# Optimization experiments

Hardware: AMD Instinct MI355X
Metric: run time of the kernel (lower is better)

## Reference

```python
import jax, jax.numpy as jnp
import numpy as np

B, C, H, W = 16, 512, 32, 32
GROUPS = 8
EPS = 1e-5


def setup_inputs() -> dict:
    key = jax.random.key(0)
    ks = jax.random.split(key, 7)
    s = 1.0 / np.sqrt(C)
    return {
        "x": jax.random.normal(ks[0], (B, C, H, W), dtype=jnp.float32),
        "gamma": jnp.ones((C,), dtype=jnp.float32),
        "beta": jnp.zeros((C,), dtype=jnp.float32),
        "w_qkv": jax.random.normal(ks[1], (3 * C, C), dtype=jnp.float32) * s,
        "b_qkv": jnp.zeros((3 * C,), dtype=jnp.float32),
        "w_proj": jax.random.normal(ks[2], (C, C), dtype=jnp.float32) * s,
        "b_proj": jnp.zeros((C,), dtype=jnp.float32),
    }


def group_norm(x, gamma, beta):
    b, c, h, w = x.shape
    xg = x.reshape(b, GROUPS, c // GROUPS, h, w)
    mean = xg.mean(axis=(2, 3, 4), keepdims=True)
    var = xg.var(axis=(2, 3, 4), keepdims=True)
    xn = ((xg - mean) * jax.lax.rsqrt(var + EPS)).reshape(b, c, h, w)
    return xn * gamma[None, :, None, None] + beta[None, :, None, None]


def reference(x, gamma, beta, w_qkv, b_qkv, w_proj, b_proj):
    b, c, h, w = x.shape
    n = h * w
    hn = group_norm(x, gamma, beta)
    # 1x1 conv == channel matmul: [3C, C] x [B, C, N] -> [B, 3C, N]
    qkv = jnp.einsum('oc,bcn->bon', w_qkv, hn.reshape(b, c, n)) + b_qkv[None, :, None]
    q, k, v = jnp.split(qkv, 3, axis=1)  # each [B, C, N]
    scale = c ** (-0.5)
    # scores [B, N, N]: q^T k
    attn = jax.nn.softmax(jnp.einsum('bcn,bcm->bnm', q, k) * scale, axis=-1)
    out = jnp.einsum('bnm,bcm->bcn', attn, v)  # [B, C, N]
    proj = jnp.einsum('oc,bcn->bon', w_proj, out) + b_proj[None, :, None]
    return x + proj.reshape(b, c, h, w)
```

## Files before the change

kernel.cpp:

```cpp
#include <hip/hip_runtime.h>


#define BATCH 16
#define CCH 512
#define NSP 1024
#define EPSV 1e-5f
#define BK 32
#define HT 4096

typedef short bf16x8 __attribute__((ext_vector_type(8)));
typedef float f32x4 __attribute__((ext_vector_type(4)));

__device__ __forceinline__ unsigned short f2bf(float f) {
    unsigned int u = __float_as_uint(f);
    u += 0x7FFF + ((u >> 16) & 1);
    return (unsigned short)(u >> 16);
}

__device__ __forceinline__ float bf2f(unsigned short h) {
    return __uint_as_float(((unsigned int)h) << 16);
}

__device__ __forceinline__ void glds16(const void* g, void* l) {
    __builtin_amdgcn_global_load_lds(
        (const __attribute__((address_space(1))) unsigned int*)g,
        (__attribute__((address_space(3))) unsigned int*)l, 16, 0, 0);
}

#define MEMF asm volatile("" ::: "memory")
#define VMW(n) asm volatile("s_waitcnt vmcnt(" #n ")" ::: "memory")

#define XCD_MAP(GX_LOG2, PER, xv, yv, bv)                 \
    const int lin_ = blockIdx.x;                          \
    const int xcd_ = lin_ & 7;                            \
    int slot_ = lin_ >> 3;                                \
    const int hi_ = (slot_ >= (PER)) ? 1 : 0;             \
    const int bv = xcd_ + 8 * hi_;                        \
    slot_ -= hi_ * (PER);                                 \
    const int xv = slot_ & ((1 << (GX_LOG2)) - 1);        \
    const int yv = slot_ >> (GX_LOG2);

__device__ __forceinline__ void gemm128_dbuf(
    const unsigned short* __restrict__ Ag, const unsigned short* __restrict__ Bg,
    int astr, int bstr, int ktot, short* L, f32x4* acc) {
    const int t = threadIdx.x;
    const int w = t >> 6, lane = t & 63;
    const int wr = (w >> 1) * 64, wc = (w & 1) * 64;
    const int fr = lane & 15;
    const int fsw = (((lane >> 4) ^ (fr & 3)) * 8);
    const int r0 = t >> 2;
    const int kc = (((t & 3) ^ (r0 & 3)) * 8);
    const unsigned short* Ap0 = Ag + (size_t)r0 * astr + kc;
    const unsigned short* Ap1 = Ag + (size_t)(r0 + 64) * astr + kc;
    const unsigned short* Bp0 = Bg + (size_t)r0 * bstr + kc;
    const unsigned short* Bp1 = Bg + (size_t)(r0 + 64) * bstr + kc;
    short* lw = L + w * 512;

#define STG(bf, kk) do {                                  \
    short* aw_ = lw + (bf) * (4 * HT);                    \
    short* bw_ = aw_ + 2 * HT;                            \
    glds16(Ap0 + (kk), aw_);                              \
    glds16(Ap1 + (kk), aw_ + 2048);                       \
    glds16(Ap0 + (kk) + 32, aw_ + HT);                    \
    glds16(Ap1 + (kk) + 32, aw_ + HT + 2048);             \
    glds16(Bp0 + (kk), bw_);                              \
    glds16(Bp1 + (kk), bw_ + 2048);                       \
    glds16(Bp0 + (kk) + 32, bw_ + HT);                    \
    glds16(Bp1 + (kk) + 32, bw_ + HT + 2048);             \
  } while (0)

#define CMP(bf) do {                                                        \
    _Pragma("unroll")                                                       \
    for (int h = 0; h < 2; h++) {                                           \
        const short* Ab_ = L + (bf) * (4 * HT) + h * HT;                    \
        const short* Bb_ = Ab_ + 2 * HT;                                    \
        bf16x8 af[4], bfr[4];                                               \
        _Pragma("unroll")                                                   \
        for (int mi = 0; mi < 4; mi++)                                      \
            af[mi] = *(const bf16x8*)(Ab_ + (wr + mi * 16 + fr) * BK + fsw);\
        _Pragma("unroll")                                                   \
        for (int ni = 0; ni < 4; ni++)                                      \
            bfr[ni] = *(const bf16x8*)(Bb_ + (wc + ni * 16 + fr) * BK + fsw);\
        _Pragma("unroll")                                                   \
        for (int mi = 0; mi < 4; mi++)                                      \
            _Pragma("unroll")                                               \
            for (int ni = 0; ni < 4; ni++)                                  \
                acc[mi * 4 + ni] = __builtin_amdgcn_mfma_f32_16x16x32_bf16( \
                    af[mi], bfr[ni], acc[mi * 4 + ni], 0, 0, 0);            \
    } } while (0)

    STG(0, 0);
    for (int k0 = 0; k0 < ktot; k0 += 128) {
        STG(1, k0 + 64);
        VMW(8);
        MEMF; __builtin_amdgcn_s_barrier();
        CMP(0);
        MEMF; __builtin_amdgcn_s_barrier();
        const int kb = (k0 + 128 < ktot) ? k0 + 128 : 0;
        STG(0, kb);
        VMW(8);
        MEMF; __builtin_amdgcn_s_barrier();
        CMP(1);
        MEMF; __builtin_amdgcn_s_barrier();
    }
    VMW(0);
#undef STG
#undef CMP
}

__device__ __forceinline__ void gemm128_sb(
    const unsigned short* __restrict__ Ag, const unsigned short* __restrict__ Bg,
    int astr, int bstr, int ktot, short* Al, short* Bl, f32x4* acc) {
    const int t = threadIdx.x;
    const int w = t >> 6, lane = t & 63;
    const int wr = (w >> 1) * 64, wc = (w & 1) * 64;
    const int fr = lane & 15;
    const int fsw = (((lane >> 4) ^ (fr & 3)) * 8);
    const int r0 = t >> 2;
    const int kc = (((t & 3) ^ (r0 & 3)) * 8);
    const unsigned short* Ap0 = Ag + (size_t)r0 * astr + kc;
    const unsigned short* Ap1 = Ag + (size_t)(r0 + 64) * astr + kc;
    const unsigned short* Bp0 = Bg + (size_t)r0 * bstr + kc;
    const unsigned short* Bp1 = Bg + (size_t)(r0 + 64) * bstr + kc;
    short* Alw = Al + w * 512;
    short* Blw = Bl + w * 512;
    for (int k0 = 0; k0 < ktot; k0 += 64) {
        glds16(Ap0 + k0, Alw);
        glds16(Ap1 + k0, Alw + 2048);
        glds16(Ap0 + k0 + 32, Alw + HT);
        glds16(Ap1 + k0 + 32, Alw + HT + 2048);
        glds16(Bp0 + k0, Blw);
        glds16(Bp1 + k0, Blw + 2048);
        glds16(Bp0 + k0 + 32, Blw + HT);
        glds16(Bp1 + k0 + 32, Blw + HT + 2048);
        __syncthreads();
#pragma unroll
        for (int h = 0; h < 2; h++) {
            const short* Ab = Al + h * HT;
            const short* Bb = Bl + h * HT;
            bf16x8 af[4], bfr[4];
#pragma unroll
            for (int mi = 0; mi < 4; mi++)
                af[mi] = *(const bf16x8*)(Ab + (wr + mi * 16 + fr) * BK + fsw);
#pragma unroll
            for (int ni = 0; ni < 4; ni++)
                bfr[ni] = *(const bf16x8*)(Bb + (wc + ni * 16 + fr) * BK + fsw);
#pragma unroll
            for (int mi = 0; mi < 4; mi++)
#pragma unroll
                for (int ni = 0; ni < 4; ni++)
                    acc[mi * 4 + ni] = __builtin_amdgcn_mfma_f32_16x16x32_bf16(
                        af[mi], bfr[ni], acc[mi * 4 + ni], 0, 0, 0);
        }
        __syncthreads();
    }
}

#define EPI_SETUP()                                          \
    const int t = threadIdx.x, lane = t & 63, w = t >> 6;    \
    const int wr = (w >> 1) * 64, wc = (w & 1) * 64;         \
    const int fr = lane & 15, rr0 = (lane >> 4) * 4;

#define ACC_INIT(acc)                                        \
    f32x4 acc[16];                                           \
    _Pragma("unroll") for (int i = 0; i < 16; i++)           \
        acc[i] = (f32x4){0.f, 0.f, 0.f, 0.f};

__global__ __launch_bounds__(256) void setup_k(
    const float* __restrict__ x, float* __restrict__ sp,
    const float* __restrict__ wa, unsigned short* __restrict__ oa, int na4,
    const float* __restrict__ wb, unsigned short* __restrict__ ob, int nb4,
    float* __restrict__ Lsum, const float* __restrict__ bqv,
    unsigned short* __restrict__ wv_t, unsigned short* __restrict__ wq_t,
    unsigned short* __restrict__ wk_t, float* __restrict__ puv,
    float* __restrict__ wu, float* __restrict__ wv_b, float* __restrict__ c0p) {
    const int t = threadIdx.x;
    const int bx = blockIdx.x;
    __shared__ float rs[4], rq[4];
    __shared__ __align__(16) unsigned short Tt[64 * 72];
    if (bx < 512) {
        const int bg = bx >> 2, q = bx & 3;
        const float4* xp = (const float4*)(x + (size_t)bg * 65536 + q * 16384);
        float s = 0.f, qq = 0.f;
#pragma unroll
        for (int i = 0; i < 16; i++) {
            float4 v = xp[t + i * 256];
            s += v.x + v.y + v.z + v.w;
            qq += v.x * v.x + v.y * v.y + v.z * v.z + v.w * v.w;
        }
#pragma unroll
        for (int off = 32; off; off >>= 1) {
            s += __shfl_down(s, off);
            qq += __shfl_down(qq, off);
        }
        const int wave = t >> 6, lane = t & 63;
        if (lane == 0) { rs[wave] = s; rq[wave] = qq; }
        __syncthreads();
        if (t == 0) {
            sp[bx * 2] = rs[0] + rs[1] + rs[2] + rs[3];
            sp[bx * 2 + 1] = rq[0] + rq[1] + rq[2] + rq[3];
        }
    } else if (bx < 1280) {
        int i = (bx - 512) * 256 + t;
        const float* src;
        unsigned short* dst;
        int j;
        if (i < na4) { src = wa; dst = oa; j = i; }
        else { j = i - na4; if (j >= nb4) return; src = wb; dst = ob; }
        float4 v = ((const float4*)src)[j];
        ushort4 o;
        o.x = f2bf(v.x); o.y = f2bf(v.y); o.z = f2bf(v.z); o.w = f2bf(v.w);
        ((ushort4*)dst)[j] = o;
    } else if (bx < 1328) {
        int i = (bx - 1280) * 256 + t;
        ((float4*)Lsum)[i] = (float4){0.f, 0.f, 0.f, 0.f};
    } else if (bx < 1520) {
        const int r = bx - 1328;
        const int sel = r >> 6;
        const int wrow = (sel == 0) ? 2 : (sel - 1);
        const float* src = wa + (size_t)wrow * 512 * 512;
        unsigned short* dst = (sel == 0) ? wv_t : ((sel == 1) ? wq_t : wk_t);
        const int to = ((r & 63) >> 3) * 64, tc = ((r & 63) & 7) * 64;
        const int ol = t >> 2, cs = t & 3;
#pragma unroll
        for (int j = 0; j < 4; j++) {
            float4 v = *(const float4*)(src + (size_t)(to + ol) * 512 + tc + cs * 16 + j * 4);
            int c = cs * 16 + j * 4;
            Tt[(c + 0) * 72 + ol] = f2bf(v.x);
            Tt[(c + 1) * 72 + ol] = f2bf(v.y);
            Tt[(c + 2) * 72 + ol] = f2bf(v.z);
            Tt[(c + 3) * 72 + ol] = f2bf(v.w);
        }
        __syncthreads();
        const int cl = t >> 2, os = t & 3;
        unsigned short* d = dst + (size_t)(tc + cl) * 512 + to + os * 16;
        const unsigned short* s2 = Tt + cl * 72 + os * 16;
        *(uint4*)d = *(const uint4*)s2;
        *(uint4*)(d + 8) = *(const uint4*)(s2 + 8);
    } else if (bx < 1522) {
        const int o = (bx - 1520) * 256 + t;
        const float* wr_ = wb + (size_t)o * 512;
        const float* bv = bqv + 1024;
        float s = 0.f;
        for (int vv = 0; vv < 512; vv += 4) {
            s += wr_[vv] * bv[vv] + wr_[vv + 1] * bv[vv + 1]
               + wr_[vv + 2] * bv[vv + 2] + wr_[vv + 3] * bv[vv + 3];
        }
        puv[o] = s;
    } else if (bx < 1526) {
        const int r = bx - 1522;
        const int isv = r >> 1;
        const int c = (r & 1) * 256 + t;
        const float* src = wa + (size_t)isv * 512 * 512;
        const float* bsr = bqv + (isv ? 0 : 512);
        float s = 0.f;
        for (int o = 0; o < 512; o++) s += src[(size_t)o * 512 + c] * bsr[o];
        (isv ? wv_b : wu)[c] = s;
    } else {
        float s = bqv[t] * bqv[512 + t] + bqv[256 + t] * bqv[768 + t];
#pragma unroll
        for (int off = 32; off; off >>= 1) s += __shfl_down(s, off);
        if ((t & 63) == 0) rs[t >> 6] = s;
        __syncthreads();
        if (t == 0) c0p[0] = rs[0] + rs[1] + rs[2] + rs[3];
    }
}

__global__ __launch_bounds__(256) void gn_tr_k(
    const float* __restrict__ x, const float* __restrict__ gamma,
    const float* __restrict__ beta, const float* __restrict__ sp,
    unsigned short* __restrict__ hn_t,
    const unsigned short* __restrict__ wp_bf, const unsigned short* __restrict__ wv_t,
    unsigned short* __restrict__ wpv_bf,
    const unsigned short* __restrict__ wk_t, const unsigned short* __restrict__ wq_t,
    unsigned short* __restrict__ wqkb,
    const float* __restrict__ wu, const float* __restrict__ wv_b,
    float* __restrict__ u, float* __restrict__ v) {
    __shared__ __align__(16) short SM[4 * HT];
    const int lin = blockIdx.x;
    const int t = threadIdx.x;
    if (lin < 16) {
        const int ot = (lin >> 2) * 128, ct2 = (lin & 3) * 128;
        ACC_INIT(acc);
        gemm128_sb(wp_bf + (size_t)ot * 512, wv_t + (size_t)ct2 * 512,
                   512, 512, 512, SM, SM + 2 * HT, acc);
        EPI_SETUP();
#pragma unroll
        for (int ni = 0; ni < 4; ni++) {
            int col = ct2 + wc + ni * 16 + fr;
#pragma unroll
            for (int mi = 0; mi < 4; mi++) {
                int row = ot + wr + mi * 16 + rr0;
#pragma unroll
                for (int r = 0; r < 4; r++)
                    wpv_bf[(size_t)(row + r) * 512 + col] = f2bf(acc[mi * 4 + ni][r]);
            }
        }
        return;
    }
    if (lin < 32) {
        const int r2 = lin - 16;
        const int jt = (r2 >> 2) * 128, ct2 = (r2 & 3) * 128;
        ACC_INIT(acc);
        gemm128_sb(wk_t + (size_t)jt * 512, wq_t + (size_t)ct2 * 512,
                   512, 512, 512, SM, SM + 2 * HT, acc);
        EPI_SETUP();
#pragma unroll
        for (int ni = 0; ni < 4; ni++) {
            int col = ct2 + wc + ni * 16 + fr;
#pragma unroll
            for (int mi = 0; mi < 4; mi++) {
                int row = jt + wr + mi * 16 + rr0;
#pragma unroll
                for (int r = 0; r < 4; r++)
                    wqkb[(size_t)(row + r) * 512 + col] = f2bf(acc[mi * 4 + ni][r]);
            }
        }
        return;
    }
    const int l2 = lin - 32;
    const int nt = l2 & 15, ct = (l2 >> 4) & 7, b = l2 >> 7;
    unsigned short* T = (unsigned short*)SM;
    const int bg = b * 8 + ct;
    float S = 0.f, Q = 0.f;
#pragma unroll
    for (int qq = 0; qq < 4; qq++) {
        S += sp[(bg * 4 + qq) * 2];
        Q += sp[(bg * 4 + qq) * 2 + 1];
    }
    const float inv = 1.f / 65536.f;
    const float mean = S * inv;
    const float rstd = rsqrtf(Q * inv - mean * mean + EPSV);
    const int cl = t >> 2, nc = t & 3;
    const int c = ct * 64 + cl;
    const float ga = gamma[c] * rstd;
    const float be = beta[c] - mean * ga;
    const float4* xp = (const float4*)(x + ((size_t)b * CCH + c) * NSP + nt * 64);
#pragma unroll
    for (int j = 0; j < 4; j++) {
        float4 vx = xp[nc * 4 + j];
        int n = nc * 16 + j * 4;
        T[(n + 0) * 72 + cl] = f2bf(vx.x * ga + be);
        T[(n + 1) * 72 + cl] = f2bf(vx.y * ga + be);
        T[(n + 2) * 72 + cl] = f2bf(vx.z * ga + be);
        T[(n + 3) * 72 + cl] = f2bf(vx.w * ga + be);
    }
    __syncthreads();
    const int nl = t >> 2, cc = t & 3;
    unsigned short* dst = hn_t + ((size_t)b * NSP + nt * 64 + nl) * CCH + ct * 64 + cc * 16;
    const unsigned short* src = T + nl * 72 + cc * 16;
    *(uint4*)dst = *(const uint4*)src;
    *(uint4*)(dst + 8) = *(const uint4*)(src + 8);
    float pu = 0.f, pv = 0.f;
    const int cbase = ct * 64 + cc * 16;
#pragma unroll
    for (int j = 0; j < 16; j++) {
        float hv = bf2f(src[j]);
        pu += hv * wu[cbase + j];
        pv += hv * wv_b[cbase + j];
    }
    pu += __shfl_xor(pu, 1); pu += __shfl_xor(pu, 2);
    pv += __shfl_xor(pv, 1); pv += __shfl_xor(pv, 2);
    if (cc == 0) {
        atomicAdd(&u[(size_t)b * NSP + nt * 64 + nl], pu);
        atomicAdd(&v[(size_t)b * NSP + nt * 64 + nl], pv);
    }
}

__global__ __launch_bounds__(256) void gemm_qku_k(
    const unsigned short* __restrict__ hn_t, const unsigned short* __restrict__ wqkb,
    const unsigned short* __restrict__ wpv_bf, const float* __restrict__ puv,
    unsigned short* __restrict__ T1, unsigned short* __restrict__ Ub) {
    __shared__ __align__(16) short L[8 * HT];
    const int lin = blockIdx.x, xcd = lin & 7;
    int slot = lin >> 3;
    const int hi = (slot >= 64) ? 1 : 0;
    const int b = xcd + 8 * hi;
    slot -= hi * 64;
    ACC_INIT(acc);
    if (slot < 32) {
        const int mt = (slot >> 2) * 128, jt = (slot & 3) * 128;
        gemm128_dbuf(hn_t + ((size_t)b * NSP + mt) * CCH,
                     wqkb + (size_t)jt * 512, CCH, 512, CCH, L, acc);
        unsigned short* Ob = T1 + (size_t)b * NSP * 512;
        EPI_SETUP();
#pragma unroll
        for (int ni = 0; ni < 4; ni++) {
            int col = jt + wc + ni * 16 + fr;
#pragma unroll
            for (int mi = 0; mi < 4; mi++) {
                int row = mt + wr + mi * 16 + rr0;
#pragma unroll
                for (int r = 0; r < 4; r++)
                    Ob[(size_t)(row + r) * 512 + col] = f2bf(acc[mi * 4 + ni][r]);
            }
        }
    } else {
        const int s2 = slot - 32;
        const int ot = (s2 >> 3) * 128, ntc = (s2 & 7) * 128;
        gemm128_dbuf(wpv_bf + (size_t)ot * 512,
                     hn_t + ((size_t)b * NSP + ntc) * CCH, 512, CCH, 512, L, acc);
        unsigned short* Ob = Ub + (size_t)b * CCH * NSP;
        EPI_SETUP();
#pragma unroll
        for (int mi = 0; mi < 4; mi++) {
            int row = ot + wr + mi * 16 + rr0;
#pragma unroll
            for (int r = 0; r < 4; r++) {
                float bias = puv[row + r];
#pragma unroll
                for (int ni = 0; ni < 4; ni++) {
                    int col = ntc + wc + ni * 16 + fr;
                    Ob[(size_t)(row + r) * NSP + col] = f2bf(acc[mi * 4 + ni][r] + bias);
                }
            }
        }
    }
}

__global__ __launch_bounds__(256) void gemm_scores_k(
    const unsigned short* __restrict__ T1, const unsigned short* __restrict__ hn_t,
    unsigned short* __restrict__ expS, float* __restrict__ Lsum,
    const float* __restrict__ u, const float* __restrict__ v,
    const float* __restrict__ c0p) {
    __shared__ __align__(16) short L[8 * HT];
    XCD_MAP(3, 64, xb, yb, b);
    const int nt = xb * 128, mt = yb * 128;
    ACC_INIT(acc);
    gemm128_dbuf(T1 + ((size_t)b * NSP + mt) * 512,
                 hn_t + ((size_t)b * NSP + nt) * CCH, 512, CCH, 512, L, acc);
    unsigned short* Ob = expS + (size_t)b * NSP * NSP;
    float* Ls = Lsum + (size_t)b * NSP;
    const float* ua = u + (size_t)b * NSP;
    const float* va = v + (size_t)b * NSP;
    const float c0v = c0p[0];
    const float scale = 0.044194173824159216f;
    EPI_SETUP();
#pragma unroll
    for (int mi = 0; mi < 4; mi++) {
#pragma unroll
        for (int r = 0; r < 4; r++) {
            const int row = mt + wr + mi * 16 + rr0 + r;
            const float ur = ua[row] + c0v;
            float rs = 0.f;
#pragma unroll
            for (int ni = 0; ni < 4; ni++) {
                int col = nt + wc + ni * 16 + fr;
                float e = __expf((acc[mi * 4 + ni][r] + ur + va[col]) * scale);
                Ob[(size_t)row * NSP + col] = f2bf(e);
                rs += e;
            }
            rs += __shfl_xor(rs, 1);
            rs += __shfl_xor(rs, 2);
            rs += __shfl_xor(rs, 4);
            rs += __shfl_xor(rs, 8);
            if (fr == 0) atomicAdd(&Ls[row], rs);
        }
    }
}

__global__ __launch_bounds__(256) void gemm_pu_k(
    const unsigned short* __restrict__ Ub, const unsigned short* __restrict__ expS,
    const float* __restrict__ Lsum, const float* __restrict__ x,
    const float* __restrict__ bp, float* __restrict__ out) {
    __shared__ __align__(16) short L[8 * HT];
    XCD_MAP(3, 32, xb, yb, b);
    const int nt = xb * 128, ot = yb * 128;
    ACC_INIT(acc);
    gemm128_dbuf(Ub + ((size_t)b * CCH + ot) * NSP,
                 expS + ((size_t)b * NSP + nt) * NSP, NSP, NSP, NSP, L, acc);
    const float* Ls = Lsum + (size_t)b * NSP;
    const size_t bbase = (size_t)b * CCH * NSP;
    EPI_SETUP();
#pragma unroll
    for (int ni = 0; ni < 4; ni++) {
        int col = nt + wc + ni * 16 + fr;
        float invl = __builtin_amdgcn_rcpf(Ls[col]);
#pragma unroll
        for (int mi = 0; mi < 4; mi++) {
            int row = ot + wr + mi * 16 + rr0;
#pragma unroll
            for (int r = 0; r < 4; r++) {
                size_t idx = bbase + (size_t)(row + r) * NSP + col;
                out[idx] = x[idx] + bp[row + r] + acc[mi * 4 + ni][r] * invl;
            }
        }
    }
}

extern "C" void kernel_launch(void* const* d_in, const int* in_sizes, int n_in,
                              void* d_out, int out_size, void* d_ws, size_t ws_size,
                              hipStream_t stream) {
    const float* x = (const float*)d_in[0];
    const float* gamma = (const float*)d_in[1];
    const float* beta = (const float*)d_in[2];
    const float* w_qkv = (const float*)d_in[3];
    const float* b_qkv = (const float*)d_in[4];
    const float* w_proj = (const float*)d_in[5];
    const float* b_proj = (const float*)d_in[6];
    float* out = (float*)d_out;

    char* ws = (char*)d_ws;
    const size_t MB = 1048576;
    const size_t KB = 1024;
    unsigned short* wqkv_bf = (unsigned short*)ws;
    unsigned short* wproj_bf = (unsigned short*)(ws + 1572864);
    float* sp = (float*)(ws + 2 * MB);
    float* Lsum = (float*)(ws + 2 * MB + 64 * KB);
    float* u = (float*)(ws + 2 * MB + 128 * KB);
    float* v = (float*)(ws + 2 * MB + 192 * KB);
    float* puv = (float*)(ws + 2 * MB + 256 * KB);
    float* wu = (float*)(ws + 2 * MB + 260 * KB);
    float* wv_b = (float*)(ws + 2 * MB + 264 * KB);
    float* c0p = (float*)(ws + 2 * MB + 268 * KB);
    unsigned short* wv_t = (unsigned short*)(ws + 2 * MB + 512 * KB);
    unsigned short* wq_t = (unsigned short*)(ws + 3 * MB);
    unsigned short* wk_t = (unsigned short*)(ws + 3 * MB + 512 * KB);
    unsigned short* hn_t = (unsigned short*)(ws + 4 * MB);
    unsigned short* T1 = (unsigned short*)(ws + 24 * MB);
    unsigned short* Ub = (unsigned short*)(ws + 60 * MB);
    unsigned short* expS = (unsigned short*)(ws + 80 * MB);
    unsigned short* wpv_bf = (unsigned short*)(ws + 114 * MB);
    unsigned short* wqkb = (unsigned short*)(ws + 115 * MB);

    setup_k<<<1527, 256, 0, stream>>>(x, sp, w_qkv, wqkv_bf, 131072,
                                      w_proj, wproj_bf, 65536, Lsum, b_qkv,
                                      wv_t, wq_t, wk_t, puv, wu, wv_b, c0p);
    gn_tr_k<<<2080, 256, 0, stream>>>(x, gamma, beta, sp, hn_t,
                                      wproj_bf, wv_t, wpv_bf,
                                      wk_t, wq_t, wqkb, wu, wv_b, u, v);
    gemm_qku_k<<<1024, 256, 0, stream>>>(hn_t, wqkb, wpv_bf, puv, T1, Ub);
    gemm_scores_k<<<1024, 256, 0, stream>>>(T1, hn_t, expS, Lsum, u, v, c0p);
    gemm_pu_k<<<512, 256, 0, stream>>>(Ub, expS, Lsum, x, b_proj, out);
}
```

Measured before the change: 208.2 us.

## Halve K-stage depth in GEMMs and use 64x128 tiles for final projection GEMM

```diff
diff --git a/kernel.cpp b/kernel.cpp
--- a/kernel.cpp
+++ b/kernel.cpp
@@ -40,7 +40,7 @@
     const int xv = slot_ & ((1 << (GX_LOG2)) - 1);        \
     const int yv = slot_ >> (GX_LOG2);
 
-__device__ __forceinline__ void gemm128_dbuf(
+__device__ __forceinline__ void gemm128_d32(
     const unsigned short* __restrict__ Ag, const unsigned short* __restrict__ Bg,
     int astr, int bstr, int ktot, short* L, f32x4* acc) {
     const int t = threadIdx.x;
@@ -57,48 +57,100 @@
     short* lw = L + w * 512;
 
 #define STG(bf, kk) do {                                  \
-    short* aw_ = lw + (bf) * (4 * HT);                    \
-    short* bw_ = aw_ + 2 * HT;                            \
-    glds16(Ap0 + (kk), aw_);                              \
-    glds16(Ap1 + (kk), aw_ + 2048);                       \
-    glds16(Ap0 + (kk) + 32, aw_ + HT);                    \
-    glds16(Ap1 + (kk) + 32, aw_ + HT + 2048);             \
-    glds16(Bp0 + (kk), bw_);                              \
-    glds16(Bp1 + (kk), bw_ + 2048);                       \
-    glds16(Bp0 + (kk) + 32, bw_ + HT);                    \
-    glds16(Bp1 + (kk) + 32, bw_ + HT + 2048);             \
+    short* p_ = lw + (bf) * 8192;                         \
+    glds16(Ap0 + (kk), p_);                               \
+    glds16(Ap1 + (kk), p_ + 2048);                        \
+    glds16(Bp0 + (kk), p_ + 4096);                        \
+    glds16(Bp1 + (kk), p_ + 6144);                        \
   } while (0)
 
 #define CMP(bf) do {                                                        \
+    const short* Ab_ = L + (bf) * 8192;                                     \
+    const short* Bb_ = Ab_ + 4096;                                          \
+    bf16x8 af[4], bfr[4];                                                   \
     _Pragma("unroll")                                                       \
-    for (int h = 0; h < 2; h++) {                                           \
-        const short* Ab_ = L + (bf) * (4 * HT) + h * HT;                    \
-        const short* Bb_ = Ab_ + 2 * HT;                                    \
-        bf16x8 af[4], bfr[4];                                               \
-        _Pragma("unroll")                                                   \
-        for (int mi = 0; mi < 4; mi++)                                      \
-            af[mi] = *(const bf16x8*)(Ab_ + (wr + mi * 16 + fr) * BK + fsw);\
+    for (int mi = 0; mi < 4; mi++)                                          \
+        af[mi] = *(const bf16x8*)(Ab_ + (wr + mi * 16 + fr) * 32 + fsw);    \
+    _Pragma("unroll")                                                       \
+    for (int ni = 0; ni < 4; ni++)                                          \
+        bfr[ni] = *(const bf16x8*)(Bb_ + (wc + ni * 16 + fr) * 32 + fsw);   \
+    _Pragma("unroll")                                                       \
+    for (int mi = 0; mi < 4; mi++)                                          \
         _Pragma("unroll")                                                   \
         for (int ni = 0; ni < 4; ni++)                                      \
-            bfr[ni] = *(const bf16x8*)(Bb_ + (wc + ni * 16 + fr) * BK + fsw);\
+            acc[mi * 4 + ni] = __builtin_amdgcn_mfma_f32_16x16x32_bf16(     \
+                af[mi], bfr[ni], acc[mi * 4 + ni], 0, 0, 0);                \
+  } while (0)
+
+    STG(0, 0);
+    for (int k0 = 0; k0 < ktot; k0 += 64) {
+        STG(1, k0 + 32);
+        VMW(4);
+        MEMF; __builtin_amdgcn_s_barrier();
+        CMP(0);
+        MEMF; __builtin_amdgcn_s_barrier();
+        const int kb = (k0 + 64 < ktot) ? k0 + 64 : 0;
+        STG(0, kb);
+        VMW(4);
+        MEMF; __builtin_amdgcn_s_barrier();
+        CMP(1);
+        MEMF; __builtin_amdgcn_s_barrier();
+    }
+    VMW(0);
+#undef STG
+#undef CMP
+}
+
+__device__ __forceinline__ void gemm64_d32(
+    const unsigned short* __restrict__ Ag, const unsigned short* __restrict__ Bg,
+    int astr, int bstr, int ktot, short* L, f32x4* acc) {
+    const int t = threadIdx.x;
+    const int w = t >> 6, lane = t & 63;
+    const int wc = w * 32;
+    const int fr = lane & 15;
+    const int fsw = (((lane >> 4) ^ (fr & 3)) * 8);
+    const int r0 = t >> 2;
+    const int kc = (((t & 3) ^ (r0 & 3)) * 8);
+    const unsigned short* Ap0 = Ag + (size_t)r0 * astr + kc;
+    const unsigned short* Bp0 = Bg + (size_t)r0 * bstr + kc;
+    const unsigned short* Bp1 = Bg + (size_t)(r0 + 64) * bstr + kc;
+    short* lw = L + w * 512;
+
+#define STG(bf, kk) do {                                  \
+    short* p_ = lw + (bf) * 6144;                         \
+    glds16(Ap0 + (kk), p_);                               \
+    glds16(Bp0 + (kk), p_ + 2048);                        \
+    glds16(Bp1 + (kk), p_ + 4096);                        \
+  } while (0)
+
+#define CMP(bf) do {                                                        \
+    const short* Ab_ = L + (bf) * 6144;                                     \
+    const short* Bb_ = Ab_ + 2048;                                          \
+    bf16x8 af[4], bfr[2];                                                   \
+    _Pragma("unroll")                                                       \
+    for (int mi = 0; mi < 4; mi++)                                          \
+        af[mi] = *(const bf16x8*)(Ab_ + (mi * 16 + fr) * 32 + fsw);         \
+    _Pragma("unroll")                                                       \
+    for (int ni = 0; ni < 2; ni++)                                          \
+        bfr[ni] = *(const bf16x8*)(Bb_ + (wc + ni * 16 + fr) * 32 + fsw);   \
+    _Pragma("unroll")                                                       \
+    for (int mi = 0; mi < 4; mi++)                                          \
         _Pragma("unroll")                                                   \
-        for (int mi = 0; mi < 4; mi++)                                      \
-            _Pragma("unroll")                                               \
-            for (int ni = 0; ni < 4; ni++)                                  \
-                acc[mi * 4 + ni] = __builtin_amdgcn_mfma_f32_16x16x32_bf16( \
-                    af[mi], bfr[ni], acc[mi * 4 + ni], 0, 0, 0);            \
-    } } while (0)
+        for (int ni = 0; ni < 2; ni++)                                      \
+            acc[mi * 2 + ni] = __builtin_amdgcn_mfma_f32_16x16x32_bf16(     \
+                af[mi], bfr[ni], acc[mi * 2 + ni], 0, 0, 0);                \
+  } while (0)
 
     STG(0, 0);
-    for (int k0 = 0; k0 < ktot; k0 += 128) {
-        STG(1, k0 + 64);
-        VMW(8);
+    for (int k0 = 0; k0 < ktot; k0 += 64) {
+        STG(1, k0 + 32);
+        VMW(3);
         MEMF; __builtin_amdgcn_s_barrier();
         CMP(0);
         MEMF; __builtin_amdgcn_s_barrier();
-        const int kb = (k0 + 128 < ktot) ? k0 + 128 : 0;
+        const int kb = (k0 + 64 < ktot) ? k0 + 64 : 0;
         STG(0, kb);
-        VMW(8);
+        VMW(3);
         MEMF; __builtin_amdgcn_s_barrier();
         CMP(1);
         MEMF; __builtin_amdgcn_s_barrier();
@@ -371,7 +423,7 @@
     const unsigned short* __restrict__ hn_t, const unsigned short* __restrict__ wqkb,
     const unsigned short* __restrict__ wpv_bf, const float* __restrict__ puv,
     unsigned short* __restrict__ T1, unsigned short* __restrict__ Ub) {
-    __shared__ __align__(16) short L[8 * HT];
+    __shared__ __align__(16) short L[16384];
     const int lin = blockIdx.x, xcd = lin & 7;
     int slot = lin >> 3;
     const int hi = (slot >= 64) ? 1 : 0;
@@ -380,8 +432,8 @@
     ACC_INIT(acc);
     if (slot < 32) {
         const int mt = (slot >> 2) * 128, jt = (slot & 3) * 128;
-        gemm128_dbuf(hn_t + ((size_t)b * NSP + mt) * CCH,
-                     wqkb + (size_t)jt * 512, CCH, 512, CCH, L, acc);
+        gemm128_d32(hn_t + ((size_t)b * NSP + mt) * CCH,
+                    wqkb + (size_t)jt * 512, CCH, 512, CCH, L, acc);
         unsigned short* Ob = T1 + (size_t)b * NSP * 512;
         EPI_SETUP();
 #pragma unroll
@@ -398,8 +450,8 @@
     } else {
         const int s2 = slot - 32;
         const int ot = (s2 >> 3) * 128, ntc = (s2 & 7) * 128;
-        gemm128_dbuf(wpv_bf + (size_t)ot * 512,
-                     hn_t + ((size_t)b * NSP + ntc) * CCH, 512, CCH, 512, L, acc);
+        gemm128_d32(wpv_bf + (size_t)ot * 512,
+                    hn_t + ((size_t)b * NSP + ntc) * CCH, 512, CCH, 512, L, acc);
         unsigned short* Ob = Ub + (size_t)b * CCH * NSP;
         EPI_SETUP();
 #pragma unroll
@@ -423,12 +475,12 @@
     unsigned short* __restrict__ expS, float* __restrict__ Lsum,
     const float* __restrict__ u, const float* __restrict__ v,
     const float* __restrict__ c0p) {
-    __shared__ __align__(16) short L[8 * HT];
+    __shared__ __align__(16) short L[16384];
     XCD_MAP(3, 64, xb, yb, b);
     const int nt = xb * 128, mt = yb * 128;
     ACC_INIT(acc);
-    gemm128_dbuf(T1 + ((size_t)b * NSP + mt) * 512,
-                 hn_t + ((size_t)b * NSP + nt) * CCH, 512, CCH, 512, L, acc);
+    gemm128_d32(T1 + ((size_t)b * NSP + mt) * 512,
+                hn_t + ((size_t)b * NSP + nt) * CCH, 512, CCH, 512, L, acc);
     unsigned short* Ob = expS + (size_t)b * NSP * NSP;
     float* Ls = Lsum + (size_t)b * NSP;
     const float* ua = u + (size_t)b * NSP;
@@ -463,26 +515,30 @@
     const unsigned short* __restrict__ Ub, const unsigned short* __restrict__ expS,
     const float* __restrict__ Lsum, const float* __restrict__ x,
     const float* __restrict__ bp, float* __restrict__ out) {
-    __shared__ __align__(16) short L[8 * HT];
-    XCD_MAP(3, 32, xb, yb, b);
-    const int nt = xb * 128, ot = yb * 128;
-    ACC_INIT(acc);
-    gemm128_dbuf(Ub + ((size_t)b * CCH + ot) * NSP,
-                 expS + ((size_t)b * NSP + nt) * NSP, NSP, NSP, NSP, L, acc);
+    __shared__ __align__(16) short L[12288];
+    XCD_MAP(3, 64, xb, yb, b);
+    const int nt = xb * 128, ot = yb * 64;
+    f32x4 acc[8];
+#pragma unroll
+    for (int i = 0; i < 8; i++) acc[i] = (f32x4){0.f, 0.f, 0.f, 0.f};
+    gemm64_d32(Ub + ((size_t)b * CCH + ot) * NSP,
+               expS + ((size_t)b * NSP + nt) * NSP, NSP, NSP, NSP, L, acc);
     const float* Ls = Lsum + (size_t)b * NSP;
     const size_t bbase = (size_t)b * CCH * NSP;
-    EPI_SETUP();
-#pragma unroll
-    for (int ni = 0; ni < 4; ni++) {
+    const int t = threadIdx.x, lane = t & 63, w = t >> 6;
+    const int fr = lane & 15, rr0 = (lane >> 4) * 4;
+    const int wc = w * 32;
+#pragma unroll
+    for (int ni = 0; ni < 2; ni++) {
         int col = nt + wc + ni * 16 + fr;
         float invl = __builtin_amdgcn_rcpf(Ls[col]);
 #pragma unroll
         for (int mi = 0; mi < 4; mi++) {
-            int row = ot + wr + mi * 16 + rr0;
+            int row = ot + mi * 16 + rr0;
 #pragma unroll
             for (int r = 0; r < 4; r++) {
                 size_t idx = bbase + (size_t)(row + r) * NSP + col;
-                out[idx] = x[idx] + bp[row + r] + acc[mi * 4 + ni][r] * invl;
+                out[idx] = x[idx] + bp[row + r] + acc[mi * 2 + ni][r] * invl;
             }
         }
     }
@@ -531,5 +587,5 @@
                                       wk_t, wq_t, wqkb, wu, wv_b, u, v);
     gemm_qku_k<<<1024, 256, 0, stream>>>(hn_t, wqkb, wpv_bf, puv, T1, Ub);
     gemm_scores_k<<<1024, 256, 0, stream>>>(T1, hn_t, expS, Lsum, u, v, c0p);
-    gemm_pu_k<<<512, 256, 0, stream>>>(Ub, expS, Lsum, x, b_proj, out);
-}
+    gemm_pu_k<<<1024, 256, 0, stream>>>(Ub, expS, Lsum, x, b_proj, out);
+}
```

Result: no change. 211.7 us (+1.7%).
